# Optimization experiments

Measured on AMD Instinct MI355X. Metric: run time of the kernel, lower is better.

## Reference

```python
import jax, jax.numpy as jnp
import numpy as np

N_NODES = 100000
N_EDGES = 1600000
IN_DIM = 128
HID = 64
N_GRAPHS = 64
OUT_DIM = 2


def setup_inputs() -> dict:
    key = jax.random.key(0)
    ks = jax.random.split(key, 16)
    x = jax.random.normal(ks[0], (N_NODES, IN_DIM), dtype=jnp.float32)
    edge_index = jax.random.randint(ks[1], (2, N_EDGES), 0, N_NODES, dtype=jnp.int64)
    batch = jnp.sort(jax.random.randint(ks[2], (N_NODES,), 0, N_GRAPHS, dtype=jnp.int64))
    def glorot(k, fan_in, fan_out):
        s = jnp.sqrt(6.0 / (fan_in + fan_out)).astype(jnp.float32)
        return jax.random.uniform(k, (fan_in, fan_out), jnp.float32, -s, s)
    return {
        "x": x, "edge_index": edge_index, "batch": batch,
        "W1": glorot(ks[3], IN_DIM, HID), "b1": jnp.zeros((HID,), jnp.float32),
        "W2": glorot(ks[4], HID, HID),   "b2": jnp.zeros((HID,), jnp.float32),
        "W3": glorot(ks[5], HID, HID),   "b3": jnp.zeros((HID,), jnp.float32),
        "Wc1": glorot(ks[6], HID, HID // 2), "bc1": jnp.zeros((HID // 2,), jnp.float32),
        "Wc2": glorot(ks[7], HID // 2, OUT_DIM), "bc2": jnp.zeros((OUT_DIM,), jnp.float32),
    }


def reference(x, edge_index, batch, W1, b1, W2, b2, W3, b3, Wc1, bc1, Wc2, bc2):
    n = x.shape[0]
    # GCNConv: add self-loops, symmetric deg^{-1/2} normalization
    loop = jnp.arange(n, dtype=edge_index.dtype)
    src = jnp.concatenate([edge_index[0], loop])  # [E+N]
    dst = jnp.concatenate([edge_index[1], loop])
    deg = jax.ops.segment_sum(jnp.ones_like(dst, dtype=x.dtype), dst, num_segments=n)
    dis = jnp.where(deg > 0, jax.lax.rsqrt(deg), 0.0)  # deg^{-1/2}
    norm = (dis[src] * dis[dst])[:, None]  # [E+N, 1]

    def conv(h, W, b):
        h = h @ W                                   # [N, F_out]
        msg = h[src] * norm                         # edge-wise gather
        return jax.ops.segment_sum(msg, dst, num_segments=n) + b  # scatter-add

    h = jax.nn.relu(conv(x, W1, b1))     # dropout is identity at inference
    h = jax.nn.relu(conv(h, W2, b2))
    h = conv(h, W3, b3)

    # global_mean_pool over batch ids
    sums = jax.ops.segment_sum(h, batch, num_segments=N_GRAPHS)
    cnts = jax.ops.segment_sum(jnp.ones((n,), h.dtype), batch, num_segments=N_GRAPHS)
    pooled = sums / jnp.maximum(cnts, 1.0)[:, None]  # [G, HID]

    # classifier MLP
    hcls = jax.nn.relu(pooled @ Wc1 + bc1)
    return hcls @ Wc2 + bc2  # [G, OUT_DIM]
```

## Files before the change

kernel.cpp:

```cpp
#include <hip/hip_runtime.h>
#include <hip/hip_bf16.h>

#define N_NODES 100000
#define N_EDGES 1600000
#define IN_DIM 128
#define HID 64
#define N_GRAPHS 64
#define OUT_DIM 2

#define NB_BUCKETS ((N_NODES + 255) / 256)
#define CHUNK 4096
#define NCHUNKS ((N_EDGES + CHUNK - 1) / CHUNK)
#define ARENA_CAP 6144


__device__ inline unsigned f2bf_rne(float f) {
    unsigned u = __float_as_uint(f);
    u += 0x7FFFu + ((u >> 16) & 1u);
    return u >> 16;
}
__device__ inline unsigned pack2(float lo, float hi) {
    return f2bf_rne(lo) | (f2bf_rne(hi) << 16);
}
__device__ inline float bf_lo(unsigned w) { return __uint_as_float(w << 16); }
__device__ inline float bf_hi(unsigned w) { return __uint_as_float(w & 0xFFFF0000u); }
__device__ inline float2 bf_pair(unsigned w) {
    return make_float2(bf_lo(w), bf_hi(w));
}
__device__ inline void acc2(float2& a, float2 b) { a.x += b.x; a.y += b.y; }
__device__ inline void accv(float2 a[4], uint4 v) {
    acc2(a[0], bf_pair(v.x)); acc2(a[1], bf_pair(v.y));
    acc2(a[2], bf_pair(v.z)); acc2(a[3], bf_pair(v.w));
}


__global__ void kb_scan(const int* __restrict__ bcount, int* __restrict__ bbase) {
    int lane = threadIdx.x;
    int carry = 0;
    for (int c = 0; c < (NB_BUCKETS + 63) / 64; ++c) {
        int idx = c * 64 + lane;
        int v = (idx < NB_BUCKETS) ? bcount[idx] : 0;
        int orig = v;
        for (int d = 1; d < 64; d <<= 1) {
            int u = __shfl_up(v, d);
            if (lane >= d) v += u;
        }
        if (idx < NB_BUCKETS) bbase[idx] = v - orig + carry;
        carry += __shfl(v, 63);
    }
    if (lane == 0) bbase[NB_BUCKETS] = carry;
}

__global__ __launch_bounds__(256) void kb_scatter(const int* __restrict__ src,
                                                  const int* __restrict__ dst,
                                                  int* __restrict__ bcount,
                                                  unsigned* __restrict__ arena) {
    __shared__ unsigned staged[CHUNK];
    __shared__ unsigned short sbuck[CHUNK];
    __shared__ int hist[NB_BUCKETS];
    __shared__ int lofs[NB_BUCKETS];
    __shared__ int lcur[NB_BUCKETS];
    __shared__ int gbase[NB_BUCKETS];
    int t = threadIdx.x;
    int lane = t & 63, wv = t >> 6;
    for (int i = t; i < NB_BUCKETS; i += 256) hist[i] = 0;
    __syncthreads();
    int chunk0 = blockIdx.x * CHUNK;
    int cN = min(CHUNK, N_EDGES - chunk0);
    for (int i = t; i < cN; i += 256) atomicAdd(&hist[dst[chunk0 + i] >> 8], 1);
    __syncthreads();
    if (wv == 0) {
        int carry = 0;
        for (int c = 0; c < (NB_BUCKETS + 63) / 64; ++c) {
            int idx = c * 64 + lane;
            int v = (idx < NB_BUCKETS) ? hist[idx] : 0;
            int orig = v;
            for (int d = 1; d < 64; d <<= 1) {
                int u = __shfl_up(v, d);
                if (lane >= d) v += u;
            }
            if (idx < NB_BUCKETS) lofs[idx] = v - orig + carry;
            carry += __shfl(v, 63);
        }
    }
    __syncthreads();
    for (int i = t; i < NB_BUCKETS; i += 256) {
        lcur[i] = lofs[i];
        gbase[i] = hist[i] ? (atomicAdd(&bcount[i], hist[i]) + i * ARENA_CAP) : 0;
    }
    __syncthreads();
    for (int i = t; i < cN; i += 256) {
        int e = chunk0 + i;
        int d = dst[e];
        int b = d >> 8;
        int lp = atomicAdd(&lcur[b], 1);
        staged[lp] = ((unsigned)src[e] << 8) | (unsigned)(d & 255);
        sbuck[lp] = (unsigned short)b;
    }
    __syncthreads();
    for (int p = t; p < cN; p += 256) {
        int b = sbuck[p];
        arena[gbase[b] + (p - lofs[b])] = staged[p];
    }
}

__global__ __launch_bounds__(256) void k_bfin(const unsigned* __restrict__ arena,
                                              const int* __restrict__ bbase,
                                              int* __restrict__ ssrc,
                                              int* __restrict__ off,
                                              float* __restrict__ dis) {
    __shared__ int cnt[256];
    __shared__ int lofs[256];
    __shared__ int lcur[256];
    int t = threadIdx.x;
    int lane = t & 63, wv = t >> 6;
    cnt[t] = 0;
    __syncthreads();
    int b = blockIdx.x;
    int lo = bbase[b];
    int cntB = bbase[b + 1] - lo;
    const unsigned* ap = arena + (size_t)b * ARENA_CAP;
    for (int e = t; e < cntB; e += 256) atomicAdd(&cnt[ap[e] & 255], 1);
    __syncthreads();
    if (wv == 0) {
        int carry = 0;
#pragma unroll
        for (int c = 0; c < 4; ++c) {
            int idx = c * 64 + lane;
            int v = cnt[idx];
            int orig = v;
            for (int d = 1; d < 64; d <<= 1) {
                int u = __shfl_up(v, d);
                if (lane >= d) v += u;
            }
            lofs[idx] = v - orig + carry;
            carry += __shfl(v, 63);
        }
    }
    __syncthreads();
    lcur[t] = lofs[t];
    int node = b * 256 + t;
    if (node < N_NODES) {
        off[node] = lo + lofs[t];
        dis[node] = rsqrtf((float)cnt[t] + 1.0f);
    }
    if (b == NB_BUCKETS - 1 && t == 0) off[N_NODES] = N_EDGES;
    __syncthreads();
    for (int e = t; e < cntB; e += 256) {
        unsigned pk = ap[e];
        int p = atomicAdd(&lcur[pk & 255u], 1);
        ssrc[lo + p] = (int)(pk >> 8);
    }
}


__global__ __launch_bounds__(256) void k_wprep(const float* __restrict__ W1,
                                               const float* __restrict__ W2,
                                               const float* __restrict__ W3,
                                               unsigned short* __restrict__ Wt1,
                                               unsigned short* __restrict__ Wt2,
                                               unsigned short* __restrict__ Wt3) {
    int t = blockIdx.x * 256 + threadIdx.x;
    if (t < 64 * 128) {
        int n = t >> 7, k = t & 127;
        Wt1[t] = (unsigned short)f2bf_rne(W1[k * 64 + n]);
    }
    if (t < 64 * 64) {
        int n = t >> 6, k = t & 63;
        Wt2[t] = (unsigned short)f2bf_rne(W2[k * 64 + n]);
        Wt3[t] = (unsigned short)f2bf_rne(W3[k * 64 + n]);
    }
}

template <int K, bool AF32>
__global__ __launch_bounds__(256) void k_gemm(const void* __restrict__ Ain,
                                              const unsigned short* __restrict__ Wt,
                                              const float* __restrict__ dis,
                                              unsigned* __restrict__ g16) {
    constexpr int PITCH = K + 8;
    constexpr int ABYTES = 2 * 64 * PITCH * 2;
    constexpr int CBYTES = 64 * 68 * 4;
    constexpr int SMEM = ABYTES > CBYTES ? ABYTES : CBYTES;
    __shared__ __align__(16) char smem[SMEM];
    short* As = (short*)smem;
    short* Bs = As + 64 * PITCH;
    float* Cs = (float*)smem;
    constexpr int CP = 68;

    int t = threadIdx.x, lane = t & 63, w = t >> 6;
    int row0 = blockIdx.x * 64;

    constexpr int UN = 64 * (K / 8);
#pragma unroll
    for (int u = t; u < UN; u += 256) {
        int r = u / (K / 8), c = u % (K / 8);
        int grow = row0 + r;
        grow = grow < N_NODES ? grow : N_NODES - 1;
        uint4 o;
        if (AF32) {
            const float* Ap = (const float*)Ain + (size_t)grow * K + c * 8;
            float4 f0 = *(const float4*)Ap;
            float4 f1 = *(const float4*)(Ap + 4);
            o.x = pack2(f0.x, f0.y); o.y = pack2(f0.z, f0.w);
            o.z = pack2(f1.x, f1.y); o.w = pack2(f1.z, f1.w);
        } else {
            o = ((const uint4*)Ain)[(size_t)grow * (K / 8) + c];
        }
        *(uint4*)&As[r * PITCH + c * 8] = o;
    }
#pragma unroll
    for (int u = t; u < UN; u += 256) {
        int n = u / (K / 8), c = u % (K / 8);
        *(uint4*)&Bs[n * PITCH + c * 8] = *(const uint4*)&Wt[n * K + c * 8];
    }
    __syncthreads();

    using frag = __attribute__((ext_vector_type(8))) short;
    using fragc = __attribute__((ext_vector_type(4))) float;
    fragc z = {0.f, 0.f, 0.f, 0.f};
    fragc acc[4] = {z, z, z, z};
    int m = lane & 15, quad = lane >> 4;
#pragma unroll
    for (int ks = 0; ks < K / 32; ++ks) {
        frag a = *(frag*)&As[(w * 16 + m) * PITCH + ks * 32 + quad * 8];
#pragma unroll
        for (int nt = 0; nt < 4; ++nt) {
            frag b = *(frag*)&Bs[(nt * 16 + m) * PITCH + ks * 32 + quad * 8];
            acc[nt] = __builtin_amdgcn_mfma_f32_16x16x32_bf16(a, b, acc[nt], 0, 0, 0);
        }
    }
    __syncthreads();
#pragma unroll
    for (int nt = 0; nt < 4; ++nt)
#pragma unroll
        for (int reg = 0; reg < 4; ++reg)
            Cs[(w * 16 + quad * 4 + reg) * CP + nt * 16 + m] = acc[nt][reg];
    __syncthreads();

    {
        int r = t >> 2, c0 = (t & 3) * 16;
        int grow = row0 + r;
        if (grow < N_NODES) {
            float dr = dis[grow];
            const float* cp = &Cs[r * CP + c0];
            uint4 o0, o1;
            o0.x = pack2(cp[0] * dr, cp[1] * dr);
            o0.y = pack2(cp[2] * dr, cp[3] * dr);
            o0.z = pack2(cp[4] * dr, cp[5] * dr);
            o0.w = pack2(cp[6] * dr, cp[7] * dr);
            o1.x = pack2(cp[8] * dr, cp[9] * dr);
            o1.y = pack2(cp[10] * dr, cp[11] * dr);
            o1.z = pack2(cp[12] * dr, cp[13] * dr);
            o1.w = pack2(cp[14] * dr, cp[15] * dr);
            ((uint4*)g16)[(size_t)grow * 8 + (c0 >> 3)] = o0;
            ((uint4*)g16)[(size_t)grow * 8 + (c0 >> 3) + 1] = o1;
        }
    }
}

__global__ __launch_bounds__(256) void k_aggr_gemm(const unsigned* __restrict__ gin,
                                                   const int* __restrict__ off,
                                                   const int* __restrict__ ssrc,
                                                   const float* __restrict__ dis,
                                                   const float* __restrict__ bias,
                                                   const unsigned short* __restrict__ Wt,
                                                   unsigned* __restrict__ gout) {
    constexpr int K = HID;
    constexpr int PITCH = K + 8;
    constexpr int ABYTES = 2 * 64 * PITCH * 2;
    constexpr int CBYTES = 64 * 68 * 4;
    constexpr int SMEM = ABYTES > CBYTES ? ABYTES : CBYTES;
    __shared__ __align__(16) char smem[SMEM];
    short* As = (short*)smem;
    short* Bs = As + 64 * PITCH;
    float* Cs = (float*)smem;
    constexpr int CP = 68;

    int t = threadIdx.x, lane = t & 63, w = t >> 6;
    int row0 = blockIdx.x * 64;
    int r8 = lane >> 3, li = lane & 7;
    const uint4* g4 = (const uint4*)gin;

#pragma unroll
    for (int u = t; u < 64 * 8; u += 256) {
        int n = u >> 3, c = u & 7;
        *(uint4*)&Bs[n * PITCH + c * 8] = *(const uint4*)&Wt[n * K + c * 8];
    }

    float4 b0 = ((const float4*)bias)[li * 2];
    float4 b1 = ((const float4*)bias)[li * 2 + 1];
#pragma unroll
    for (int half = 0; half < 2; ++half) {
        int r = w * 8 + r8 + half * 32;
        int row = row0 + r;
        int crow = row < N_NODES ? row : N_NODES - 1;
        float2 acc[4] = {make_float2(0.f, 0.f), make_float2(0.f, 0.f),
                         make_float2(0.f, 0.f), make_float2(0.f, 0.f)};
        int lo = off[crow], hi = off[crow + 1];
        int e = lo;
        for (; e + 3 < hi; e += 4) {
            unsigned o0 = (unsigned)ssrc[e] * 8u + (unsigned)li;
            unsigned o1 = (unsigned)ssrc[e + 1] * 8u + (unsigned)li;
            unsigned o2 = (unsigned)ssrc[e + 2] * 8u + (unsigned)li;
            unsigned o3 = (unsigned)ssrc[e + 3] * 8u + (unsigned)li;
            uint4 v0 = g4[o0], v1 = g4[o1], v2 = g4[o2], v3 = g4[o3];
            accv(acc, v0); accv(acc, v1); accv(acc, v2); accv(acc, v3);
        }
        for (; e < hi; ++e) {
            uint4 v = g4[(unsigned)ssrc[e] * 8u + (unsigned)li];
            accv(acc, v);
        }
        uint4 sv = g4[(unsigned)crow * 8u + (unsigned)li];
        float2 sp[4] = {bf_pair(sv.x), bf_pair(sv.y), bf_pair(sv.z), bf_pair(sv.w)};
        float dr = dis[crow];
        float bb[8] = {b0.x, b0.y, b0.z, b0.w, b1.x, b1.y, b1.z, b1.w};
        float o[8];
#pragma unroll
        for (int j = 0; j < 4; ++j) {
            o[2 * j]     = fmaxf(dr * (acc[j].x + sp[j].x) + bb[2 * j], 0.f);
            o[2 * j + 1] = fmaxf(dr * (acc[j].y + sp[j].y) + bb[2 * j + 1], 0.f);
        }
        uint4 hv;
        hv.x = pack2(o[0], o[1]);
        hv.y = pack2(o[2], o[3]);
        hv.z = pack2(o[4], o[5]);
        hv.w = pack2(o[6], o[7]);
        *(uint4*)&As[r * PITCH + li * 8] = hv;
    }
    __syncthreads();

    using frag = __attribute__((ext_vector_type(8))) short;
    using fragc = __attribute__((ext_vector_type(4))) float;
    fragc z = {0.f, 0.f, 0.f, 0.f};
    fragc acc[4] = {z, z, z, z};
    int m = lane & 15, quad = lane >> 4;
#pragma unroll
    for (int ks = 0; ks < K / 32; ++ks) {
        frag a = *(frag*)&As[(w * 16 + m) * PITCH + ks * 32 + quad * 8];
#pragma unroll
        for (int nt = 0; nt < 4; ++nt) {
            frag b = *(frag*)&Bs[(nt * 16 + m) * PITCH + ks * 32 + quad * 8];
            acc[nt] = __builtin_amdgcn_mfma_f32_16x16x32_bf16(a, b, acc[nt], 0, 0, 0);
        }
    }
    __syncthreads();
#pragma unroll
    for (int nt = 0; nt < 4; ++nt)
#pragma unroll
        for (int reg = 0; reg < 4; ++reg)
            Cs[(w * 16 + quad * 4 + reg) * CP + nt * 16 + m] = acc[nt][reg];
    __syncthreads();
    {
        int r = t >> 2, c0 = (t & 3) * 16;
        int grow = row0 + r;
        if (grow < N_NODES) {
            float dr = dis[grow];
            const float* cp = &Cs[r * CP + c0];
            uint4 o0, o1;
            o0.x = pack2(cp[0] * dr, cp[1] * dr);
            o0.y = pack2(cp[2] * dr, cp[3] * dr);
            o0.z = pack2(cp[4] * dr, cp[5] * dr);
            o0.w = pack2(cp[6] * dr, cp[7] * dr);
            o1.x = pack2(cp[8] * dr, cp[9] * dr);
            o1.y = pack2(cp[10] * dr, cp[11] * dr);
            o1.z = pack2(cp[12] * dr, cp[13] * dr);
            o1.w = pack2(cp[14] * dr, cp[15] * dr);
            ((uint4*)gout)[(size_t)grow * 8 + (c0 >> 3)] = o0;
            ((uint4*)gout)[(size_t)grow * 8 + (c0 >> 3) + 1] = o1;
        }
    }
}

template <bool RELU>
__global__ __launch_bounds__(256) void k_aggr(const unsigned* __restrict__ g16,
                                              const int* __restrict__ off,
                                              const int* __restrict__ ssrc,
                                              const float* __restrict__ dis,
                                              const float* __restrict__ bias,
                                              unsigned* __restrict__ h16) {
    int lane = threadIdx.x & 63, wv = threadIdx.x >> 6;
    int r8 = lane >> 3;
    int li = lane & 7;
    int row = blockIdx.x * 32 + wv * 8 + r8;
    if (row >= N_NODES) return;
    const uint4* g4 = (const uint4*)g16;
    float2 acc[4] = {make_float2(0.f, 0.f), make_float2(0.f, 0.f),
                     make_float2(0.f, 0.f), make_float2(0.f, 0.f)};
    int lo = off[row], hi = off[row + 1];
    int e = lo;
    for (; e + 3 < hi; e += 4) {
        unsigned o0 = (unsigned)ssrc[e] * 8u + (unsigned)li;
        unsigned o1 = (unsigned)ssrc[e + 1] * 8u + (unsigned)li;
        unsigned o2 = (unsigned)ssrc[e + 2] * 8u + (unsigned)li;
        unsigned o3 = (unsigned)ssrc[e + 3] * 8u + (unsigned)li;
        uint4 v0 = g4[o0], v1 = g4[o1], v2 = g4[o2], v3 = g4[o3];
        accv(acc, v0); accv(acc, v1); accv(acc, v2); accv(acc, v3);
    }
    for (; e < hi; ++e) {
        uint4 v = g4[(unsigned)ssrc[e] * 8u + (unsigned)li];
        accv(acc, v);
    }
    unsigned base = (unsigned)row * 8u + (unsigned)li;
    uint4 sv = g4[base];
    float2 sp[4] = {bf_pair(sv.x), bf_pair(sv.y), bf_pair(sv.z), bf_pair(sv.w)};
    float dr = dis[row];
    float4 b0 = ((const float4*)bias)[li * 2];
    float4 b1 = ((const float4*)bias)[li * 2 + 1];
    float bb[8] = {b0.x, b0.y, b0.z, b0.w, b1.x, b1.y, b1.z, b1.w};
    float o[8];
#pragma unroll
    for (int j = 0; j < 4; ++j) {
        o[2 * j]     = dr * (acc[j].x + sp[j].x) + bb[2 * j];
        o[2 * j + 1] = dr * (acc[j].y + sp[j].y) + bb[2 * j + 1];
    }
    if (RELU) {
#pragma unroll
        for (int j = 0; j < 8; ++j) o[j] = fmaxf(o[j], 0.f);
    }
    uint4 wvo;
    wvo.x = pack2(o[0], o[1]);
    wvo.y = pack2(o[2], o[3]);
    wvo.z = pack2(o[4], o[5]);
    wvo.w = pack2(o[6], o[7]);
    ((uint4*)h16)[base] = wvo;
}


__global__ __launch_bounds__(256) void k_pool1(const unsigned short* __restrict__ h16,
                                               const int* __restrict__ batch,
                                               float* __restrict__ sums) {
    int lane = threadIdx.x & 63, wv = threadIdx.x >> 6;
    int node0 = blockIdx.x * 256 + wv * 64;
    int node1 = min(node0 + 64, N_NODES);
    float acc = 0.f;
    int cur = -1;
    for (int i = node0; i < node1; ++i) {
        int bi = batch[i];
        if (bi != cur) {
            if (cur >= 0) atomicAdd(&sums[cur * HID + lane], acc);
            acc = 0.f;
            cur = bi;
        }
        unsigned u = h16[(size_t)i * HID + lane];
        acc += __uint_as_float(u << 16);
    }
    if (cur >= 0) atomicAdd(&sums[cur * HID + lane], acc);
}

__device__ inline int lower_bound_batch(const int* batch, int key) {
    int lo = 0, hi = N_NODES;
    while (lo < hi) {
        int mid = (lo + hi) >> 1;
        if (batch[mid] < key) lo = mid + 1;
        else hi = mid;
    }
    return lo;
}

__global__ __launch_bounds__(256) void k_cls(const float* __restrict__ sums,
                                             const int* __restrict__ batch,
                                             const float* __restrict__ Wc1,
                                             const float* __restrict__ bc1,
                                             const float* __restrict__ Wc2,
                                             const float* __restrict__ bc2,
                                             float* __restrict__ out) {
    __shared__ float pooled[N_GRAPHS][HID];
    __shared__ float hc[N_GRAPHS][HID / 2];
    __shared__ float cnts[N_GRAPHS];
    int t = threadIdx.x;
    if (t < N_GRAPHS) {
        int lo = lower_bound_batch(batch, t);
        int hi = lower_bound_batch(batch, t + 1);
        cnts[t] = fmaxf((float)(hi - lo), 1.0f);
    }
    __syncthreads();
    for (int idx = t; idx < N_GRAPHS * HID; idx += 256) {
        int gi = idx >> 6;
        pooled[gi][idx & 63] = sums[idx] / cnts[gi];
    }
    __syncthreads();
    for (int idx = t; idx < N_GRAPHS * (HID / 2); idx += 256) {
        int gi = idx >> 5, f = idx & 31;
        float a = bc1[f];
#pragma unroll
        for (int k = 0; k < HID; ++k) a = fmaf(pooled[gi][k], Wc1[k * (HID / 2) + f], a);
        hc[gi][f] = fmaxf(a, 0.f);
    }
    __syncthreads();
    for (int idx = t; idx < N_GRAPHS * OUT_DIM; idx += 256) {
        int gi = idx >> 1, f = idx & 1;
        float a = bc2[f];
#pragma unroll
        for (int k = 0; k < HID / 2; ++k) a = fmaf(hc[gi][k], Wc2[k * OUT_DIM + f], a);
        out[gi * OUT_DIM + f] = a;
    }
}


extern "C" void kernel_launch(void* const* d_in, const int* in_sizes, int n_in,
                              void* d_out, int out_size, void* d_ws, size_t ws_size,
                              hipStream_t stream) {
    const float* x    = (const float*)d_in[0];
    const int*   eidx = (const int*)d_in[1];
    const int*   batch= (const int*)d_in[2];
    const float* W1 = (const float*)d_in[3];  const float* b1 = (const float*)d_in[4];
    const float* W2 = (const float*)d_in[5];  const float* b2 = (const float*)d_in[6];
    const float* W3 = (const float*)d_in[7];  const float* b3 = (const float*)d_in[8];
    const float* Wc1 = (const float*)d_in[9];  const float* bc1 = (const float*)d_in[10];
    const float* Wc2 = (const float*)d_in[11]; const float* bc2 = (const float*)d_in[12];
    float* out = (float*)d_out;

    const int* esrc = eidx;
    const int* edst = eidx + N_EDGES;

    size_t o = 0;
    auto alloc = [&](size_t bytes) {
        void* p = (char*)d_ws + o;
        o += (bytes + 255) & ~(size_t)255;
        return p;
    };
    int*            bcount = (int*)alloc((size_t)NB_BUCKETS * 4);
    int*            bbase  = (int*)alloc((size_t)(NB_BUCKETS + 1) * 4);
    float*          dis    = (float*)alloc((size_t)N_NODES * 4);
    unsigned*       arena  = (unsigned*)alloc((size_t)NB_BUCKETS * ARENA_CAP * 4);
    int*            ssrc   = (int*)alloc((size_t)N_EDGES * 4);
    int*            off    = (int*)alloc((size_t)(N_NODES + 1) * 4);
    unsigned*       gA     = (unsigned*)alloc((size_t)N_NODES * HID * 2);
    unsigned*       gB     = (unsigned*)alloc((size_t)N_NODES * HID * 2);
    unsigned short* Wt1    = (unsigned short*)alloc((size_t)64 * 128 * 2);
    unsigned short* Wt2    = (unsigned short*)alloc((size_t)64 * 64 * 2);
    unsigned short* Wt3    = (unsigned short*)alloc((size_t)64 * 64 * 2);
    float*          sums   = (float*)alloc((size_t)N_GRAPHS * HID * 4);
    (void)ws_size;

    const int TB = 256;
    int gridG = (N_NODES + 63) / 64;
    int gridR = (N_NODES + 31) / 32;

    hipMemsetAsync(bcount, 0, (size_t)NB_BUCKETS * 4, stream);
    hipMemsetAsync(sums, 0, (size_t)N_GRAPHS * HID * 4, stream);
    k_wprep<<<32, TB, 0, stream>>>(W1, W2, W3, Wt1, Wt2, Wt3);
    kb_scatter<<<NCHUNKS, TB, 0, stream>>>(esrc, edst, bcount, arena);
    kb_scan<<<1, 64, 0, stream>>>(bcount, bbase);
    k_bfin<<<NB_BUCKETS, TB, 0, stream>>>(arena, bbase, ssrc, off, dis);

    k_gemm<IN_DIM, true><<<gridG, TB, 0, stream>>>(x, Wt1, dis, gA);

    k_aggr_gemm<<<gridG, TB, 0, stream>>>(gA, off, ssrc, dis, b1, Wt2, gB);

    k_aggr_gemm<<<gridG, TB, 0, stream>>>(gB, off, ssrc, dis, b2, Wt3, gA);

    k_aggr<false><<<gridR, TB, 0, stream>>>(gA, off, ssrc, dis, b3, gB);

    k_pool1<<<NB_BUCKETS, TB, 0, stream>>>((const unsigned short*)gB, batch, sums);
    k_cls<<<1, TB, 0, stream>>>(sums, batch, Wc1, bc1, Wc2, bc2, out);
}
```

Baseline: 320.7 us.

## Fuse final aggregation with mean pooling and widen aggregate-GEMM blocks to 512 threads

The last GCN aggregation now accumulates its output directly into per-block shared-memory graph sums and flushes them to global memory with atomics. This drops the intermediate layer-3 bf16 write, its re-read, and the separate pooling kernel. The aggregate+GEMM kernel now runs 512 threads per block, one node row per wave group instead of two sequential halves, and splits the MFMA N-tiles across waves. The gain is more memory-level parallelism in the gather. The cost is shared-memory atomics in the pool and more cross-block global atomics on the sums.

```diff
diff --git a/kernel.cpp b/kernel.cpp
--- a/kernel.cpp
+++ b/kernel.cpp
@@ -258,7 +258,7 @@
     }
 }
 
-__global__ __launch_bounds__(256) void k_aggr_gemm(const unsigned* __restrict__ gin,
+__global__ __launch_bounds__(512) void k_aggr_gemm(const unsigned* __restrict__ gin,
                                                    const int* __restrict__ off,
                                                    const int* __restrict__ ssrc,
                                                    const float* __restrict__ dis,
@@ -281,19 +281,17 @@
     int r8 = lane >> 3, li = lane & 7;
     const uint4* g4 = (const uint4*)gin;
 
-#pragma unroll
-    for (int u = t; u < 64 * 8; u += 256) {
-        int n = u >> 3, c = u & 7;
+    {
+        int n = t >> 3, c = t & 7;
         *(uint4*)&Bs[n * PITCH + c * 8] = *(const uint4*)&Wt[n * K + c * 8];
     }
 
-    float4 b0 = ((const float4*)bias)[li * 2];
-    float4 b1 = ((const float4*)bias)[li * 2 + 1];
-#pragma unroll
-    for (int half = 0; half < 2; ++half) {
-        int r = w * 8 + r8 + half * 32;
+    {
+        int r = w * 8 + r8;
         int row = row0 + r;
         int crow = row < N_NODES ? row : N_NODES - 1;
+        float4 b0 = ((const float4*)bias)[li * 2];
+        float4 b1 = ((const float4*)bias)[li * 2 + 1];
         float2 acc[4] = {make_float2(0.f, 0.f), make_float2(0.f, 0.f),
                          make_float2(0.f, 0.f), make_float2(0.f, 0.f)};
         int lo = off[crow], hi = off[crow + 1];
@@ -332,120 +330,101 @@
     using frag = __attribute__((ext_vector_type(8))) short;
     using fragc = __attribute__((ext_vector_type(4))) float;
     fragc z = {0.f, 0.f, 0.f, 0.f};
-    fragc acc[4] = {z, z, z, z};
+    fragc acc[2] = {z, z};
     int m = lane & 15, quad = lane >> 4;
+    int mt = w & 3, nh = w >> 2;
 #pragma unroll
     for (int ks = 0; ks < K / 32; ++ks) {
-        frag a = *(frag*)&As[(w * 16 + m) * PITCH + ks * 32 + quad * 8];
-#pragma unroll
-        for (int nt = 0; nt < 4; ++nt) {
+        frag a = *(frag*)&As[(mt * 16 + m) * PITCH + ks * 32 + quad * 8];
+#pragma unroll
+        for (int n2 = 0; n2 < 2; ++n2) {
+            int nt = nh * 2 + n2;
             frag b = *(frag*)&Bs[(nt * 16 + m) * PITCH + ks * 32 + quad * 8];
-            acc[nt] = __builtin_amdgcn_mfma_f32_16x16x32_bf16(a, b, acc[nt], 0, 0, 0);
-        }
-    }
-    __syncthreads();
-#pragma unroll
-    for (int nt = 0; nt < 4; ++nt)
+            acc[n2] = __builtin_amdgcn_mfma_f32_16x16x32_bf16(a, b, acc[n2], 0, 0, 0);
+        }
+    }
+    __syncthreads();
+#pragma unroll
+    for (int n2 = 0; n2 < 2; ++n2)
 #pragma unroll
         for (int reg = 0; reg < 4; ++reg)
-            Cs[(w * 16 + quad * 4 + reg) * CP + nt * 16 + m] = acc[nt][reg];
+            Cs[(mt * 16 + quad * 4 + reg) * CP + (nh * 2 + n2) * 16 + m] = acc[n2][reg];
     __syncthreads();
     {
-        int r = t >> 2, c0 = (t & 3) * 16;
+        int r = t >> 3, c0 = (t & 7) * 8;
         int grow = row0 + r;
         if (grow < N_NODES) {
             float dr = dis[grow];
             const float* cp = &Cs[r * CP + c0];
-            uint4 o0, o1;
-            o0.x = pack2(cp[0] * dr, cp[1] * dr);
-            o0.y = pack2(cp[2] * dr, cp[3] * dr);
-            o0.z = pack2(cp[4] * dr, cp[5] * dr);
-            o0.w = pack2(cp[6] * dr, cp[7] * dr);
-            o1.x = pack2(cp[8] * dr, cp[9] * dr);
-            o1.y = pack2(cp[10] * dr, cp[11] * dr);
-            o1.z = pack2(cp[12] * dr, cp[13] * dr);
-            o1.w = pack2(cp[14] * dr, cp[15] * dr);
-            ((uint4*)gout)[(size_t)grow * 8 + (c0 >> 3)] = o0;
-            ((uint4*)gout)[(size_t)grow * 8 + (c0 >> 3) + 1] = o1;
-        }
-    }
-}
-
-template <bool RELU>
-__global__ __launch_bounds__(256) void k_aggr(const unsigned* __restrict__ g16,
-                                              const int* __restrict__ off,
-                                              const int* __restrict__ ssrc,
-                                              const float* __restrict__ dis,
-                                              const float* __restrict__ bias,
-                                              unsigned* __restrict__ h16) {
-    int lane = threadIdx.x & 63, wv = threadIdx.x >> 6;
-    int r8 = lane >> 3;
-    int li = lane & 7;
-    int row = blockIdx.x * 32 + wv * 8 + r8;
-    if (row >= N_NODES) return;
-    const uint4* g4 = (const uint4*)g16;
-    float2 acc[4] = {make_float2(0.f, 0.f), make_float2(0.f, 0.f),
-                     make_float2(0.f, 0.f), make_float2(0.f, 0.f)};
-    int lo = off[row], hi = off[row + 1];
-    int e = lo;
-    for (; e + 3 < hi; e += 4) {
-        unsigned o0 = (unsigned)ssrc[e] * 8u + (unsigned)li;
-        unsigned o1 = (unsigned)ssrc[e + 1] * 8u + (unsigned)li;
-        unsigned o2 = (unsigned)ssrc[e + 2] * 8u + (unsigned)li;
-        unsigned o3 = (unsigned)ssrc[e + 3] * 8u + (unsigned)li;
-        uint4 v0 = g4[o0], v1 = g4[o1], v2 = g4[o2], v3 = g4[o3];
-        accv(acc, v0); accv(acc, v1); accv(acc, v2); accv(acc, v3);
-    }
-    for (; e < hi; ++e) {
-        uint4 v = g4[(unsigned)ssrc[e] * 8u + (unsigned)li];
-        accv(acc, v);
-    }
-    unsigned base = (unsigned)row * 8u + (unsigned)li;
-    uint4 sv = g4[base];
-    float2 sp[4] = {bf_pair(sv.x), bf_pair(sv.y), bf_pair(sv.z), bf_pair(sv.w)};
-    float dr = dis[row];
-    float4 b0 = ((const float4*)bias)[li * 2];
-    float4 b1 = ((const float4*)bias)[li * 2 + 1];
-    float bb[8] = {b0.x, b0.y, b0.z, b0.w, b1.x, b1.y, b1.z, b1.w};
-    float o[8];
-#pragma unroll
-    for (int j = 0; j < 4; ++j) {
-        o[2 * j]     = dr * (acc[j].x + sp[j].x) + bb[2 * j];
-        o[2 * j + 1] = dr * (acc[j].y + sp[j].y) + bb[2 * j + 1];
-    }
-    if (RELU) {
-#pragma unroll
-        for (int j = 0; j < 8; ++j) o[j] = fmaxf(o[j], 0.f);
-    }
-    uint4 wvo;
-    wvo.x = pack2(o[0], o[1]);
-    wvo.y = pack2(o[2], o[3]);
-    wvo.z = pack2(o[4], o[5]);
-    wvo.w = pack2(o[6], o[7]);
-    ((uint4*)h16)[base] = wvo;
-}
-
-
-__global__ __launch_bounds__(256) void k_pool1(const unsigned short* __restrict__ h16,
-                                               const int* __restrict__ batch,
-                                               float* __restrict__ sums) {
-    int lane = threadIdx.x & 63, wv = threadIdx.x >> 6;
-    int node0 = blockIdx.x * 256 + wv * 64;
-    int node1 = min(node0 + 64, N_NODES);
-    float acc = 0.f;
-    int cur = -1;
-    for (int i = node0; i < node1; ++i) {
-        int bi = batch[i];
-        if (bi != cur) {
-            if (cur >= 0) atomicAdd(&sums[cur * HID + lane], acc);
-            acc = 0.f;
-            cur = bi;
-        }
-        unsigned u = h16[(size_t)i * HID + lane];
-        acc += __uint_as_float(u << 16);
-    }
-    if (cur >= 0) atomicAdd(&sums[cur * HID + lane], acc);
-}
+            uint4 o;
+            o.x = pack2(cp[0] * dr, cp[1] * dr);
+            o.y = pack2(cp[2] * dr, cp[3] * dr);
+            o.z = pack2(cp[4] * dr, cp[5] * dr);
+            o.w = pack2(cp[6] * dr, cp[7] * dr);
+            ((uint4*)gout)[(size_t)grow * 8 + (t & 7)] = o;
+        }
+    }
+}
+
+__global__ __launch_bounds__(256) void k_aggr_pool(const unsigned* __restrict__ g16,
+                                                   const int* __restrict__ off,
+                                                   const int* __restrict__ ssrc,
+                                                   const float* __restrict__ dis,
+                                                   const float* __restrict__ bias,
+                                                   const int* __restrict__ batch,
+                                                   float* __restrict__ sums) {
+    __shared__ float pacc[N_GRAPHS][HID];
+    int t = threadIdx.x;
+    int lane = t & 63, wv = t >> 6;
+    int r8 = lane >> 3, li = lane & 7;
+    int row0 = blockIdx.x * 32;
+    int row = row0 + wv * 8 + r8;
+    bool valid = row < N_NODES;
+    int gmin = batch[min(row0, N_NODES - 1)];
+    int gmax = batch[min(row0 + 31, N_NODES - 1)];
+    int gspan = gmax - gmin + 1;
+    for (int idx = t; idx < gspan * HID; idx += 256)
+        pacc[gmin + (idx >> 6)][idx & 63] = 0.f;
+    __syncthreads();
+    if (valid) {
+        const uint4* g4 = (const uint4*)g16;
+        float2 acc[4] = {make_float2(0.f, 0.f), make_float2(0.f, 0.f),
+                         make_float2(0.f, 0.f), make_float2(0.f, 0.f)};
+        int lo = off[row], hi = off[row + 1];
+        int e = lo;
+        for (; e + 3 < hi; e += 4) {
+            unsigned o0 = (unsigned)ssrc[e] * 8u + (unsigned)li;
+            unsigned o1 = (unsigned)ssrc[e + 1] * 8u + (unsigned)li;
+            unsigned o2 = (unsigned)ssrc[e + 2] * 8u + (unsigned)li;
+            unsigned o3 = (unsigned)ssrc[e + 3] * 8u + (unsigned)li;
+            uint4 v0 = g4[o0], v1 = g4[o1], v2 = g4[o2], v3 = g4[o3];
+            accv(acc, v0); accv(acc, v1); accv(acc, v2); accv(acc, v3);
+        }
+        for (; e < hi; ++e) {
+            uint4 v = g4[(unsigned)ssrc[e] * 8u + (unsigned)li];
+            accv(acc, v);
+        }
+        unsigned base = (unsigned)row * 8u + (unsigned)li;
+        uint4 sv = g4[base];
+        float2 sp[4] = {bf_pair(sv.x), bf_pair(sv.y), bf_pair(sv.z), bf_pair(sv.w)};
+        float dr = dis[row];
+        float4 b0 = ((const float4*)bias)[li * 2];
+        float4 b1 = ((const float4*)bias)[li * 2 + 1];
+        float bb[8] = {b0.x, b0.y, b0.z, b0.w, b1.x, b1.y, b1.z, b1.w};
+        float* pg = &pacc[batch[row]][li * 8];
+#pragma unroll
+        for (int j = 0; j < 4; ++j) {
+            atomicAdd(&pg[2 * j],     dr * (acc[j].x + sp[j].x) + bb[2 * j]);
+            atomicAdd(&pg[2 * j + 1], dr * (acc[j].y + sp[j].y) + bb[2 * j + 1]);
+        }
+    }
+    __syncthreads();
+    for (int idx = t; idx < gspan * HID; idx += 256) {
+        int g = gmin + (idx >> 6);
+        atomicAdd(&sums[g * HID + (idx & 63)], pacc[g][idx & 63]);
+    }
+}
+
 
 __device__ inline int lower_bound_batch(const int* batch, int key) {
     int lo = 0, hi = N_NODES;
@@ -535,7 +514,7 @@
 
     const int TB = 256;
     int gridG = (N_NODES + 63) / 64;
-    int gridR = (N_NODES + 31) / 32;
+    int gridP = (N_NODES + 31) / 32;
 
     hipMemsetAsync(bcount, 0, (size_t)NB_BUCKETS * 4, stream);
     hipMemsetAsync(sums, 0, (size_t)N_GRAPHS * HID * 4, stream);
@@ -546,12 +525,11 @@
 
     k_gemm<IN_DIM, true><<<gridG, TB, 0, stream>>>(x, Wt1, dis, gA);
 
-    k_aggr_gemm<<<gridG, TB, 0, stream>>>(gA, off, ssrc, dis, b1, Wt2, gB);
-
-    k_aggr_gemm<<<gridG, TB, 0, stream>>>(gB, off, ssrc, dis, b2, Wt3, gA);
-
-    k_aggr<false><<<gridR, TB, 0, stream>>>(gA, off, ssrc, dis, b3, gB);
-
-    k_pool1<<<NB_BUCKETS, TB, 0, stream>>>((const unsigned short*)gB, batch, sums);
+    k_aggr_gemm<<<gridG, 512, 0, stream>>>(gA, off, ssrc, dis, b1, Wt2, gB);
+
+    k_aggr_gemm<<<gridG, 512, 0, stream>>>(gB, off, ssrc, dis, b2, Wt3, gA);
+
+    k_aggr_pool<<<gridP, TB, 0, stream>>>(gA, off, ssrc, dis, b3, batch, sums);
+
     k_cls<<<1, TB, 0, stream>>>(sums, batch, Wc1, bc1, Wc2, bc2, out);
 }
```

After: 302.5 us. 1.06x faster.
